# Optimization experiments

Measured on AMD Instinct MI355X. Metric: run time of the kernel, lower is better.

Reference implementation:

```python
import jax, jax.numpy as jnp
import numpy as np

B, T, C, H, M, R = 2, 2048, 768, 6, 3072, 320
D = C // H  # head_dim = 128


def setup_inputs() -> dict:
    key = jax.random.key(0)
    ks = jax.random.split(key, 11)
    s = 0.02
    return {
        "x": jax.random.normal(ks[0], (B, T, C), jnp.float32),
        "forward_memory": jax.random.normal(ks[1], (B, M, C), jnp.float32),
        "reverse_memory": jax.random.normal(ks[2], (B, R, C), jnp.float32),
        "ctrl": jax.random.uniform(ks[3], (5,), jnp.float32),
        "Wq": jax.random.normal(ks[4], (C, C), jnp.float32) * s,
        "Wk": jax.random.normal(ks[5], (C, C), jnp.float32) * s,
        "Wv": jax.random.normal(ks[6], (C, C), jnp.float32) * s,
        "Wo": jax.random.normal(ks[7], (C, C), jnp.float32) * s,
        "Wc": jax.random.normal(ks[8], (C, 5), jnp.float32) * 1e-4,  # ctrl_init_scale
        "Wg": jax.random.normal(ks[9], (H, C), jnp.float32) * s,
        "bg": jnp.full((H,), -1.0, jnp.float32),  # gate_bias_init
    }


def reference(x, forward_memory, reverse_memory, ctrl, Wq, Wk, Wv, Wo, Wc, Wg, bg):
    Bx, Tx, Cx = x.shape
    Hx = bg.shape[0]
    Dx = Cx // Hx
    # query with control-vector fusion (ctrl broadcast to every token)
    q = x @ Wq.T + ctrl @ Wc.T  # [B,T,C]
    # concat local tokens with forward+reverse memory, project K/V once
    kv_in = jnp.concatenate([x, forward_memory, reverse_memory], axis=1)  # [B,S,C]
    k = kv_in @ Wk.T
    v = kv_in @ Wv.T

    def heads(t):
        return t.reshape(Bx, -1, Hx, Dx).transpose(0, 2, 1, 3)  # [B,H,*,D]

    qh, kh, vh = heads(q), heads(k), heads(v)
    S = kh.shape[2]
    scores = jnp.einsum("bhtd,bhsd->bhts", qh, kh) * (Dx ** -0.5)
    # causal mask over local block only; memory columns always visible
    causal = jnp.triu(jnp.ones((Tx, Tx), bool), 1)
    mask = jnp.concatenate([causal, jnp.zeros((Tx, S - Tx), bool)], axis=1)
    scores = jnp.where(mask, jnp.float32(-1e30), scores)
    w = jax.nn.softmax(scores, axis=-1)  # [B,H,T,S]
    # split attention output into local and memory contributions
    local = jnp.einsum("bhts,bhsd->bhtd", w[..., :Tx], vh[:, :, :Tx])
    mem = jnp.einsum("bhts,bhsd->bhtd", w[..., Tx:], vh[:, :, Tx:])
    # per-head sigmoid gate on the memory path, computed from the fused query
    gate = jax.nn.sigmoid(q @ Wg.T + bg)  # [B,T,H]
    gate = gate.transpose(0, 2, 1)[..., None]  # [B,H,T,1]
    out = local + gate * mem
    out = out.transpose(0, 2, 1, 3).reshape(Bx, Tx, Cx)
    return out @ Wo.T
```

## Files before the change

### kernel.cpp

```cpp
#include <hip/hip_runtime.h>


typedef unsigned short u16;
typedef unsigned int   u32;
typedef __bf16 bf16x8 __attribute__((ext_vector_type(8)));
typedef float  f32x4  __attribute__((ext_vector_type(4)));

#define B_ 2
#define T_ 2048
#define C_ 768
#define H_ 6
#define D_ 128
#define M_ 3072
#define R_ 320
#define S_ 5440
#define BT_ 4096
#define BS_ 10880
#define NS_ 4
#define NMEM_ 53

#define GLDS(src, dst) __builtin_amdgcn_global_load_lds( \
    (const __attribute__((address_space(1))) void*)(src), \
    (__attribute__((address_space(3))) void*)(dst), 16, 0, 0)

#define MFMA16(a, b, c) __builtin_amdgcn_mfma_f32_16x16x32_bf16((a), (b), (c), 0, 0, 0)

__device__ __forceinline__ float b2f(u16 u) {
  union { u32 i; float f; } c; c.i = ((u32)u) << 16; return c.f;
}
__device__ __forceinline__ u16 f2b(float f) {
  union { float f; u32 i; } c; c.f = f;
  return (u16)((c.i + 0x7FFFu + ((c.i >> 16) & 1u)) >> 16);
}

__global__ __launch_bounds__(256) void k_cast4(const float* __restrict__ s0,
                                               const float* __restrict__ s1,
                                               const float* __restrict__ s2,
                                               const float* __restrict__ s3,
                                               u16* __restrict__ d0,
                                               u16* __restrict__ d1,
                                               u16* __restrict__ d2,
                                               u16* __restrict__ d3) {
  const float* src = (blockIdx.y == 0) ? s0 : (blockIdx.y == 1) ? s1
                   : (blockIdx.y == 2) ? s2 : s3;
  u16* dst = (blockIdx.y == 0) ? d0 : (blockIdx.y == 1) ? d1
           : (blockIdx.y == 2) ? d2 : d3;
  int i = (blockIdx.x * 256 + threadIdx.x) * 4;
  float4 v = *(const float4*)(src + i);
  u16 o[4] = { f2b(v.x), f2b(v.y), f2b(v.z), f2b(v.w) };
  *(ushort4*)(dst + i) = *(ushort4*)o;
}

__global__ __launch_bounds__(256) void k_concat(const float* __restrict__ x,
                                                const float* __restrict__ fm,
                                                const float* __restrict__ rm,
                                                u16* __restrict__ kv) {
  long long i = ((long long)blockIdx.x * 256 + threadIdx.x) * 8;
  if (i >= (long long)BS_ * C_) return;
  int row = (int)(i / C_);
  int col = (int)(i - (long long)row * C_);
  int b = row / S_, s = row - b * S_;
  const float* src;
  if (s < T_)           src = x  + (size_t)(b * T_ + s) * C_ + col;
  else if (s < T_ + M_) src = fm + (size_t)(b * M_ + (s - T_)) * C_ + col;
  else                  src = rm + (size_t)(b * R_ + (s - T_ - M_)) * C_ + col;
  float4 a0 = *(const float4*)src;
  float4 a1 = *(const float4*)(src + 4);
  u16 o[8] = { f2b(a0.x), f2b(a0.y), f2b(a0.z), f2b(a0.w),
               f2b(a1.x), f2b(a1.y), f2b(a1.z), f2b(a1.w) };
  *(uint4*)(kv + i) = *(uint4*)o;
}

template<bool F32OUT, bool QCBIAS>
__global__ __launch_bounds__(256) void k_gemm(const u16* __restrict__ A,
                                              const u16* __restrict__ W,
                                              const float* __restrict__ ctrl,
                                              const float* __restrict__ Wc,
                                              void* __restrict__ outv,
                                              int rows, int rowShift, int bstride) {
  __shared__ __align__(16) u16 As[3][128 * 32];
  __shared__ __align__(16) u16 Bs[3][128 * 32];
  const int t = threadIdx.x;
  const int lane = t & 63, wv = t >> 6;
  const int wr = (wv >> 1) * 64, wc = (wv & 1) * 64;
  const int fr = lane & 15, fq = lane >> 4;
  const int rowTile = blockIdx.x * 128;
  const int colTile = blockIdx.y * 128;

  f32x4 acc[4][4] = {};

  const int e0 = t * 8;
  const int e1 = (256 + t) * 8;
  const int r0 = e0 >> 5, c0 = e0 & 31;
  const int r1 = e1 >> 5, c1 = e1 & 31;

  int gr0 = rowTile + r0; if (gr0 >= rows) gr0 = rows - 1;
  int gr1 = rowTile + r1; if (gr1 >= rows) gr1 = rows - 1;
  const int msk = (1 << rowShift) - 1;
  const size_t pr0 = (size_t)(gr0 >> rowShift) * bstride + (gr0 & msk);
  const size_t pr1 = (size_t)(gr1 >> rowShift) * bstride + (gr1 & msk);
  const u16* gaB0 = A + pr0 * C_ + c0;
  const u16* gaB1 = A + pr1 * C_ + c1;
  const u16* gbB0 = W + (size_t)(colTile + r0) * C_ + c0;
  const u16* gbB1 = W + (size_t)(colTile + r1) * C_ + c1;
  const int aOff0 = (wv * 64) * 8, aOff1 = (256 + wv * 64) * 8;

#define STAGE_G(bi, kt) do { \
    GLDS(gaB0 + (kt), &As[bi][aOff0]); \
    GLDS(gaB1 + (kt), &As[bi][aOff1]); \
    GLDS(gbB0 + (kt), &Bs[bi][aOff0]); \
    GLDS(gbB1 + (kt), &Bs[bi][aOff1]); } while (0)

  STAGE_G(0, 0);
  STAGE_G(1, 32);
  int cur = 0;

  for (int kt = 0; kt < C_; kt += 32) {
    int nx2 = cur + 2; if (nx2 >= 3) nx2 -= 3;
    if (kt + 64 < C_) {
      STAGE_G(nx2, kt + 64);
      asm volatile("s_waitcnt vmcnt(8)" ::: "memory");
    } else if (kt + 32 < C_) {
      asm volatile("s_waitcnt vmcnt(4)" ::: "memory");
    } else {
      asm volatile("s_waitcnt vmcnt(0)" ::: "memory");
    }
    __builtin_amdgcn_s_barrier();

    bf16x8 af[4], bfr[4];
#pragma unroll
    for (int i = 0; i < 4; ++i) af[i]  = *(const bf16x8*)&As[cur][(wr + i * 16 + fr) * 32 + fq * 8];
#pragma unroll
    for (int i = 0; i < 4; ++i) bfr[i] = *(const bf16x8*)&Bs[cur][(wc + i * 16 + fr) * 32 + fq * 8];
#pragma unroll
    for (int mi = 0; mi < 4; ++mi)
#pragma unroll
      for (int ni = 0; ni < 4; ++ni)
        acc[mi][ni] = MFMA16(af[mi], bfr[ni], acc[mi][ni]);
    __builtin_amdgcn_s_barrier();
    cur = (cur == 2) ? 0 : cur + 1;
  }
#undef STAGE_G

#pragma unroll
  for (int mi = 0; mi < 4; ++mi) {
#pragma unroll
    for (int ni = 0; ni < 4; ++ni) {
      int cc = colTile + wc + ni * 16 + fr;
      float bb = 0.f;
      if (QCBIAS) {
#pragma unroll
        for (int j = 0; j < 5; ++j) bb += ctrl[j] * Wc[cc * 5 + j];
      }
#pragma unroll
      for (int j = 0; j < 4; ++j) {
        int rr = rowTile + wr + mi * 16 + fq * 4 + j;
        if (rr < rows) {
          float val = acc[mi][ni][j] + bb;
          if (F32OUT) ((float*)outv)[(size_t)rr * C_ + cc] = val;
          else        ((u16*)outv)[(size_t)rr * C_ + cc] = f2b(val);
        }
      }
    }
  }
}

__global__ __launch_bounds__(256, 2) void k_gemmKV(const u16* __restrict__ kvb,
                                                   const u16* __restrict__ Wk,
                                                   const u16* __restrict__ Wv,
                                                   u16* __restrict__ kb,
                                                   u16* __restrict__ vt) {
  __shared__ __align__(16) u16 As[2][128 * 32];
  __shared__ __align__(16) u16 Ks2[2][128 * 32];
  __shared__ __align__(16) u16 Vs2[2][128 * 32];
  const int t = threadIdx.x;
  const int lane = t & 63, wv = t >> 6;
  const int wr = (wv >> 1) * 64, wc = (wv & 1) * 64;
  const int fr = lane & 15, fq = lane >> 4;
  const int rowTile = blockIdx.x * 128;
  const int colTile = blockIdx.y * 128;

  f32x4 accK[4][4] = {};
  f32x4 accV[4][4] = {};

  const int e0 = t * 8;
  const int e1 = (256 + t) * 8;
  const int r0 = e0 >> 5, c0 = e0 & 31;
  const int r1 = e1 >> 5, c1 = e1 & 31;

  const u16* gaB0 = kvb + (size_t)(rowTile + r0) * C_ + c0;
  const u16* gaB1 = kvb + (size_t)(rowTile + r1) * C_ + c1;
  const u16* gkB0 = Wk + (size_t)(colTile + r0) * C_ + c0;
  const u16* gkB1 = Wk + (size_t)(colTile + r1) * C_ + c1;
  const u16* gvB0 = Wv + (size_t)(colTile + r0) * C_ + c0;
  const u16* gvB1 = Wv + (size_t)(colTile + r1) * C_ + c1;
  const int aOff0 = (wv * 64) * 8, aOff1 = (256 + wv * 64) * 8;

#define STAGE_KV(bi, kt) do { \
    GLDS(gaB0 + (kt), &As[bi][aOff0]); \
    GLDS(gaB1 + (kt), &As[bi][aOff1]); \
    GLDS(gkB0 + (kt), &Ks2[bi][aOff0]); \
    GLDS(gkB1 + (kt), &Ks2[bi][aOff1]); \
    GLDS(gvB0 + (kt), &Vs2[bi][aOff0]); \
    GLDS(gvB1 + (kt), &Vs2[bi][aOff1]); } while (0)

  STAGE_KV(0, 0);
  int cur = 0;

  for (int kt = 0; kt < C_; kt += 32) {
    if (kt + 32 < C_) {
      STAGE_KV(cur ^ 1, kt + 32);
      asm volatile("s_waitcnt vmcnt(6)" ::: "memory");
    } else {
      asm volatile("s_waitcnt vmcnt(0)" ::: "memory");
    }
    __builtin_amdgcn_s_barrier();

    bf16x8 af[4], wkf[4], wvf[4];
#pragma unroll
    for (int i = 0; i < 4; ++i) af[i]  = *(const bf16x8*)&As[cur][(wr + i * 16 + fr) * 32 + fq * 8];
#pragma unroll
    for (int i = 0; i < 4; ++i) wkf[i] = *(const bf16x8*)&Ks2[cur][(wc + i * 16 + fr) * 32 + fq * 8];
#pragma unroll
    for (int i = 0; i < 4; ++i) wvf[i] = *(const bf16x8*)&Vs2[cur][(wc + i * 16 + fr) * 32 + fq * 8];
#pragma unroll
    for (int mi = 0; mi < 4; ++mi)
#pragma unroll
      for (int ni = 0; ni < 4; ++ni) {
        accK[mi][ni] = MFMA16(af[mi], wkf[ni], accK[mi][ni]);
        accV[mi][ni] = MFMA16(wvf[mi], af[ni], accV[mi][ni]);
      }
    __builtin_amdgcn_s_barrier();
    cur ^= 1;
  }
#undef STAGE_KV

#pragma unroll
  for (int mi = 0; mi < 4; ++mi) {
#pragma unroll
    for (int ni = 0; ni < 4; ++ni) {
      int cc = colTile + wc + ni * 16 + fr;
#pragma unroll
      for (int j = 0; j < 4; ++j) {
        int rr = rowTile + wr + mi * 16 + fq * 4 + j;
        kb[(size_t)rr * C_ + cc] = f2b(accK[mi][ni][j]);
      }
    }
  }
#pragma unroll
  for (int mi = 0; mi < 4; ++mi) {
#pragma unroll
    for (int ni = 0; ni < 4; ++ni) {
      int sg = rowTile + wr + ni * 16 + fr;
      int b = sg / S_, s = sg - b * S_;
#pragma unroll
      for (int j = 0; j < 4; ++j) {
        int cc = colTile + wc + mi * 16 + fq * 4 + j;
        vt[((size_t)(b * C_ + cc)) * S_ + s] = f2b(accV[mi][ni][j]);
      }
    }
  }
}

__global__ __launch_bounds__(256) void k_gate(const u16* __restrict__ q,
                                              const float* __restrict__ Wg,
                                              const float* __restrict__ bg,
                                              float* __restrict__ gate) {
  int gid = blockIdx.x * 4 + (threadIdx.x >> 6);
  int lane = threadIdx.x & 63;
  int h = gid % H_;
  int bt = gid / H_;
  const u16* qrow = q + (size_t)bt * C_;
  const float* wrow = Wg + (size_t)h * C_;
  float a = 0.f;
#pragma unroll
  for (int i = 0; i < 12; ++i) {
    int e = i * 64 + lane;
    a += b2f(qrow[e]) * wrow[e];
  }
#pragma unroll
  for (int off = 1; off < 64; off <<= 1) a += __shfl_xor(a, off);
  if (lane == 0) {
    float xg = a + bg[h];
    int b = bt / T_, tt = bt - b * T_;
    gate[((size_t)b * H_ + h) * T_ + tt] = 1.f / (1.f + __expf(-xg));
  }
}

__global__ __launch_bounds__(256, 2) void k_attn10(const u16* __restrict__ q,
                                                   const u16* __restrict__ kk,
                                                   const u16* __restrict__ vt,
                                                   const float* __restrict__ gate,
                                                   u16* __restrict__ pacc0,
                                                   u16* __restrict__ pacc1,
                                                   u16* __restrict__ pacc2,
                                                   u16* __restrict__ pacc3,
                                                   float* __restrict__ pl) {
  __shared__ __align__(16) u16 Ks[2][64 * 128];
  __shared__ __align__(16) u16 Vs[128 * 64];
  __shared__ __align__(16) u16 Pb[4][32 * 64];

  const int bh = blockIdx.x;
  const int b = bh / H_, h = bh - b * H_;
  const int y = 15 - blockIdx.y;
  const int c = blockIdx.z;
  const int wv = threadIdx.x >> 6, lane = threadIdx.x & 63;
  const int fr = lane & 15, fq = lane >> 4;
  const int qbase = y * 128 + wv * 32;
  char* Pc = (char*)Pb[wv];

  const u16* Qh = q + (size_t)(b * T_ + qbase) * C_ + h * D_;
  const float* gh = gate + ((size_t)b * H_ + h) * T_ + qbase;

  const int kR = lane >> 4, kCb = (lane & 15) * 16;
  const u16* kS[4];
#pragma unroll
  for (int j = 0; j < 4; ++j) {
    int row = wv * 16 + j * 4 + kR;
    kS[j] = kk + (size_t)(b * S_ + row) * C_ + h * D_ + ((kCb ^ ((row & 7) << 4)) >> 1);
  }
  const int vR = lane >> 3, vCb = (lane & 7) * 16;
  const u16* vS[4];
#pragma unroll
  for (int j = 0; j < 4; ++j) {
    int row = wv * 32 + j * 8 + vR;
    vS[j] = vt + ((size_t)b * C_ + h * D_ + row) * S_ + ((vCb ^ ((row & 7) << 4)) >> 1);
  }

#define STAGE_K(buf, s) do { _Pragma("unroll") \
    for (int j = 0; j < 4; ++j) \
      GLDS(kS[j] + (size_t)(s) * C_, &Ks[buf][(wv * 16 + j * 4) * 128]); } while (0)
#define STAGE_V(s) do { _Pragma("unroll") \
    for (int j = 0; j < 4; ++j) \
      GLDS(vS[j] + (s), &Vs[(wv * 32 + j * 8) * 64]); } while (0)

  bf16x8 qf0[4], qf1[4];
#pragma unroll
  for (int kc = 0; kc < 4; ++kc) {
    qf0[kc] = *(const bf16x8*)&Qh[(size_t)fr * C_ + kc * 32 + fq * 8];
    qf1[kc] = *(const bf16x8*)&Qh[(size_t)(16 + fr) * C_ + kc * 32 + fq * 8];
  }

  f32x4 acc0[8] = {}, acc1[8] = {};
  f32x4 accL0 = {}, accM0 = {}, accL1 = {}, accM1 = {};
  float g0[4], lg0[4], g1[4], lg1[4];
#pragma unroll
  for (int r = 0; r < 4; ++r) {
    g0[r] = gh[fq * 4 + r];      lg0[r] = __log2f(g0[r]);
    g1[r] = gh[16 + fq * 4 + r]; lg1[r] = __log2f(g1[r]);
  }

  const __bf16 one_h = (__bf16)1.0f;
  bf16x8 ones = { one_h, one_h, one_h, one_h, one_h, one_h, one_h, one_h };

  const float scl = 0.08838834764831845f * 1.4426950408889634f;
  const int xk = (fr & 7) << 4;

  const int nloc = 2 * y + 2;
  const int ntot = nloc + NMEM_;
  auto s_of = [&](int i) { return (i < nloc) ? i * 64 : T_ + (i - nloc) * 64; };

  STAGE_K(0, s_of(c));
  int cur = 0;

  for (int i = c; i < ntot; i += NS_) {
    const int s0 = s_of(i);
    const bool haveNext = (i + NS_ < ntot);
    STAGE_V(s0);
    if (haveNext) {
      STAGE_K(cur ^ 1, s_of(i + NS_));
      asm volatile("s_waitcnt vmcnt(8)" ::: "memory");
    } else {
      asm volatile("s_waitcnt vmcnt(4)" ::: "memory");
    }
    __builtin_amdgcn_s_barrier();

    const bool loc = (i < nloc);
    const bool maskedStep = loc && (s0 + 63 > qbase);
    const bool skip = loc && (s0 > qbase + 31);

    bf16x8 pa00, pa01, pa10, pa11;
    if (!skip) {
      f32x4 sc0[4] = {{}, {}, {}, {}};
      f32x4 sc1[4] = {{}, {}, {}, {}};
#pragma unroll
      for (int quad = 0; quad < 4; ++quad) {
        const u16* Krow = &Ks[cur][(quad * 16 + fr) * 128];
#pragma unroll
        for (int kc = 0; kc < 4; ++kc) {
          bf16x8 kf = *(const bf16x8*)&Krow[((kc * 64 + fq * 16) ^ xk) >> 1];
          sc0[quad] = MFMA16(qf0[kc], kf, sc0[quad]);
          sc1[quad] = MFMA16(qf1[kc], kf, sc1[quad]);
        }
      }
      if (maskedStep) {
#pragma unroll
        for (int quad = 0; quad < 4; ++quad)
#pragma unroll
          for (int r = 0; r < 4; ++r) {
            int col = s0 + quad * 16 + fr;
            if (col > qbase + fq * 4 + r)      sc0[quad][r] = -1.0e30f;
            if (col > qbase + 16 + fq * 4 + r) sc1[quad][r] = -1.0e30f;
          }
      }
#pragma unroll
      for (int quad = 0; quad < 4; ++quad)
#pragma unroll
        for (int r = 0; r < 4; ++r) {
          int row = fq * 4 + r;
          int cb = (quad * 32 + fr * 2) ^ ((row & 7) << 4);
          float ca0 = loc ? 0.f : lg0[r];
          float ca1 = loc ? 0.f : lg1[r];
          *(__bf16*)(Pc + row * 128 + cb) =
              (__bf16)exp2f(fmaf(sc0[quad][r], scl, ca0));
          *(__bf16*)(Pc + (16 + row) * 128 + cb) =
              (__bf16)exp2f(fmaf(sc1[quad][r], scl, ca1));
        }
      __builtin_amdgcn_wave_barrier();
      pa00 = *(const bf16x8*)(Pc + fr * 128 + ((fq * 16) ^ xk));
      pa01 = *(const bf16x8*)(Pc + fr * 128 + ((64 + fq * 16) ^ xk));
      pa10 = *(const bf16x8*)(Pc + (16 + fr) * 128 + ((fq * 16) ^ xk));
      pa11 = *(const bf16x8*)(Pc + (16 + fr) * 128 + ((64 + fq * 16) ^ xk));
    }
    if (haveNext) asm volatile("s_waitcnt vmcnt(4)" ::: "memory");
    else          asm volatile("s_waitcnt vmcnt(0)" ::: "memory");
    __builtin_amdgcn_s_barrier();
    if (!skip) {
#pragma unroll
      for (int nt = 0; nt < 8; ++nt) {
        const u16* Vrow = &Vs[(nt * 16 + fr) * 64];
        bf16x8 vf0 = *(const bf16x8*)&Vrow[((fq * 16) ^ xk) >> 1];
        bf16x8 vf1 = *(const bf16x8*)&Vrow[((64 + fq * 16) ^ xk) >> 1];
        acc0[nt] = MFMA16(pa00, vf0, acc0[nt]);
        acc0[nt] = MFMA16(pa01, vf1, acc0[nt]);
        acc1[nt] = MFMA16(pa10, vf0, acc1[nt]);
        acc1[nt] = MFMA16(pa11, vf1, acc1[nt]);
      }
      if (loc) {
        accL0 = MFMA16(pa00, ones, accL0);
        accL0 = MFMA16(pa01, ones, accL0);
        accL1 = MFMA16(pa10, ones, accL1);
        accL1 = MFMA16(pa11, ones, accL1);
      } else {
        accM0 = MFMA16(pa00, ones, accM0);
        accM0 = MFMA16(pa01, ones, accM0);
        accM1 = MFMA16(pa10, ones, accM1);
        accM1 = MFMA16(pa11, ones, accM1);
      }
    }
    __builtin_amdgcn_s_barrier();
    cur ^= 1;
  }
#undef STAGE_K
#undef STAGE_V

  u16* pb = (c == 0) ? pacc0 : (c == 1) ? pacc1 : (c == 2) ? pacc2 : pacc3;
  const size_t rowb = (size_t)bh * T_ + qbase;
#pragma unroll
  for (int nt = 0; nt < 8; ++nt)
#pragma unroll
    for (int r = 0; r < 4; ++r) {
      ((__bf16*)pb)[(rowb + fq * 4 + r) * D_ + nt * 16 + fr] = (__bf16)acc0[nt][r];
      ((__bf16*)pb)[(rowb + 16 + fq * 4 + r) * D_ + nt * 16 + fr] = (__bf16)acc1[nt][r];
    }
  if (fr == 0) {
    const size_t plb = ((size_t)c * (B_ * H_) + bh) * T_ + qbase;
#pragma unroll
    for (int r = 0; r < 4; ++r) {
      pl[plb + fq * 4 + r]      = accL0[r] + accM0[r] / g0[r];
      pl[plb + 16 + fq * 4 + r] = accL1[r] + accM1[r] / g1[r];
    }
  }
}

__global__ __launch_bounds__(256) void k_combine(const u16* __restrict__ pacc0,
                                                 const u16* __restrict__ pacc1,
                                                 const u16* __restrict__ pacc2,
                                                 const u16* __restrict__ pacc3,
                                                 const float* __restrict__ pl,
                                                 u16* __restrict__ ao) {
  const int row = blockIdx.x * 4 + (threadIdx.x >> 6);
  const int lane = threadIdx.x & 63;
  const int bh = row >> 11, t = row & (T_ - 1);
  const int b = bh / H_, h = bh - b * H_;

  float L = pl[(size_t)bh * T_ + t]
          + pl[((size_t)(B_ * H_) + bh) * T_ + t]
          + pl[((size_t)(2 * B_ * H_) + bh) * T_ + t]
          + pl[((size_t)(3 * B_ * H_) + bh) * T_ + t];
  float inv = 1.f / L;
  const size_t rb = ((size_t)bh * T_ + t) * D_ + lane * 2;
  u32 v0 = *(const u32*)&pacc0[rb];
  u32 v1 = *(const u32*)&pacc1[rb];
  u32 v2 = *(const u32*)&pacc2[rb];
  u32 v3 = *(const u32*)&pacc3[rb];
  float o0 = b2f((u16)(v0 & 0xFFFF)) + b2f((u16)(v1 & 0xFFFF))
           + b2f((u16)(v2 & 0xFFFF)) + b2f((u16)(v3 & 0xFFFF));
  float o1 = b2f((u16)(v0 >> 16)) + b2f((u16)(v1 >> 16))
           + b2f((u16)(v2 >> 16)) + b2f((u16)(v3 >> 16));
  u16 o[2] = { f2b(o0 * inv), f2b(o1 * inv) };
  *(u32*)&ao[((size_t)(b * T_ + t)) * C_ + h * D_ + lane * 2] = *(u32*)o;
}

extern "C" void kernel_launch(void* const* d_in, const int* in_sizes, int n_in,
                              void* d_out, int out_size, void* d_ws, size_t ws_size,
                              hipStream_t stream) {
  const float* x   = (const float*)d_in[0];
  const float* fm  = (const float*)d_in[1];
  const float* rm  = (const float*)d_in[2];
  const float* ctl = (const float*)d_in[3];
  const float* Wq  = (const float*)d_in[4];
  const float* Wk  = (const float*)d_in[5];
  const float* Wv  = (const float*)d_in[6];
  const float* Wo  = (const float*)d_in[7];
  const float* Wc  = (const float*)d_in[8];
  const float* Wg  = (const float*)d_in[9];
  const float* bg  = (const float*)d_in[10];
  float* outp = (float*)d_out;

  char* ws = (char*)d_ws;
  float* gate = (float*)(ws + 4096);
  u16* qb    = (u16*)(ws + 102400);
  u16* kv    = (u16*)(ws + 6393856);
  u16* pacc0 = (u16*)(ws + 6393856);
  u16* pacc1 = (u16*)(ws + 12685312);
  u16* kb    = (u16*)(ws + 23105536);
  u16* vt    = (u16*)(ws + 39817216);
  u16* ao    = (u16*)(ws + 39817216);
  u16* pacc2 = (u16*)(ws + 56528896);
  u16* pacc3 = (u16*)(ws + 62820352);
  float* pl  = (float*)(ws + 69111808);
  u16* Wqb   = (u16*)(ws + 69505024);
  u16* Wkb   = (u16*)(ws + 70684672);
  u16* Wvb   = (u16*)(ws + 71864320);
  u16* Wob   = (u16*)(ws + 73043968);

  k_cast4<<<dim3(576, 4), dim3(256), 0, stream>>>(Wq, Wk, Wv, Wo,
                                                  Wqb, Wkb, Wvb, Wob);
  k_concat<<<dim3(4080), dim3(256), 0, stream>>>(x, fm, rm, kv);
  k_gemm<false, true><<<dim3(32, 6), dim3(256), 0, stream>>>(
      kv, Wqb, ctl, Wc, qb, BT_, 11, S_);
  k_gemmKV<<<dim3(85, 6), dim3(256), 0, stream>>>(kv, Wkb, Wvb, kb, vt);
  k_gate<<<dim3(6144), dim3(256), 0, stream>>>(qb, Wg, bg, gate);
  k_attn10<<<dim3(B_ * H_, 16, NS_), dim3(256), 0, stream>>>(
      qb, kb, vt, gate, pacc0, pacc1, pacc2, pacc3, pl);
  k_combine<<<dim3(6144), dim3(256), 0, stream>>>(pacc0, pacc1, pacc2, pacc3, pl, ao);
  k_gemm<true, false><<<dim3(32, 6), dim3(256), 0, stream>>>(
      ao, Wob, nullptr, nullptr, outp, BT_, 30, 0);
}
```

Measured before the change: 206.2 us.

## Load V fragments directly from global into registers instead of staging through LDS

New measurement: 338.0 us. +63.9%, slower.

```diff
diff --git a/kernel.cpp b/kernel.cpp
--- a/kernel.cpp
+++ b/kernel.cpp
@@ -287,7 +287,7 @@
   }
 }
 
-__global__ __launch_bounds__(256, 2) void k_attn10(const u16* __restrict__ q,
+__global__ __launch_bounds__(256, 2) void k_attn11(const u16* __restrict__ q,
                                                    const u16* __restrict__ kk,
                                                    const u16* __restrict__ vt,
                                                    const float* __restrict__ gate,
@@ -297,7 +297,6 @@
                                                    u16* __restrict__ pacc3,
                                                    float* __restrict__ pl) {
   __shared__ __align__(16) u16 Ks[2][64 * 128];
-  __shared__ __align__(16) u16 Vs[128 * 64];
   __shared__ __align__(16) u16 Pb[4][32 * 64];
 
   const int bh = blockIdx.x;
@@ -319,20 +318,11 @@
     int row = wv * 16 + j * 4 + kR;
     kS[j] = kk + (size_t)(b * S_ + row) * C_ + h * D_ + ((kCb ^ ((row & 7) << 4)) >> 1);
   }
-  const int vR = lane >> 3, vCb = (lane & 7) * 16;
-  const u16* vS[4];
-#pragma unroll
-  for (int j = 0; j < 4; ++j) {
-    int row = wv * 32 + j * 8 + vR;
-    vS[j] = vt + ((size_t)b * C_ + h * D_ + row) * S_ + ((vCb ^ ((row & 7) << 4)) >> 1);
-  }
+  const u16* vG = vt + ((size_t)b * C_ + h * D_ + fr) * S_ + fq * 8;
 
 #define STAGE_K(buf, s) do { _Pragma("unroll") \
     for (int j = 0; j < 4; ++j) \
       GLDS(kS[j] + (size_t)(s) * C_, &Ks[buf][(wv * 16 + j * 4) * 128]); } while (0)
-#define STAGE_V(s) do { _Pragma("unroll") \
-    for (int j = 0; j < 4; ++j) \
-      GLDS(vS[j] + (s), &Vs[(wv * 32 + j * 8) * 64]); } while (0)
 
   bf16x8 qf0[4], qf1[4];
 #pragma unroll
@@ -366,23 +356,29 @@
   for (int i = c; i < ntot; i += NS_) {
     const int s0 = s_of(i);
     const bool haveNext = (i + NS_ < ntot);
-    STAGE_V(s0);
-    if (haveNext) {
-      STAGE_K(cur ^ 1, s_of(i + NS_));
-      asm volatile("s_waitcnt vmcnt(8)" ::: "memory");
-    } else {
-      asm volatile("s_waitcnt vmcnt(4)" ::: "memory");
-    }
-    __builtin_amdgcn_s_barrier();
-
     const bool loc = (i < nloc);
     const bool maskedStep = loc && (s0 + 63 > qbase);
     const bool skip = loc && (s0 > qbase + 31);
 
-    bf16x8 pa00, pa01, pa10, pa11;
+    bf16x8 vfa[8], vfb[8];
     if (!skip) {
-      f32x4 sc0[4] = {{}, {}, {}, {}};
-      f32x4 sc1[4] = {{}, {}, {}, {}};
+#pragma unroll
+      for (int nt = 0; nt < 8; ++nt) {
+        vfa[nt] = *(const bf16x8*)&vG[(size_t)(nt * 16) * S_ + s0];
+        vfb[nt] = *(const bf16x8*)&vG[(size_t)(nt * 16) * S_ + s0 + 32];
+      }
+    }
+    if (haveNext) {
+      STAGE_K(cur ^ 1, s_of(i + NS_));
+      asm volatile("s_waitcnt vmcnt(20)" ::: "memory");
+    } else {
+      asm volatile("s_waitcnt vmcnt(16)" ::: "memory");
+    }
+    __builtin_amdgcn_s_barrier();
+
+    f32x4 sc0[4] = {{}, {}, {}, {}};
+    f32x4 sc1[4] = {{}, {}, {}, {}};
+    if (!skip) {
 #pragma unroll
       for (int quad = 0; quad < 4; ++quad) {
         const u16* Krow = &Ks[cur][(quad * 16 + fr) * 128];
@@ -393,6 +389,9 @@
           sc1[quad] = MFMA16(qf1[kc], kf, sc1[quad]);
         }
       }
+    }
+    __builtin_amdgcn_s_barrier();
+    if (!skip) {
       if (maskedStep) {
 #pragma unroll
         for (int quad = 0; quad < 4; ++quad)
@@ -417,24 +416,18 @@
               (__bf16)exp2f(fmaf(sc1[quad][r], scl, ca1));
         }
       __builtin_amdgcn_wave_barrier();
-      pa00 = *(const bf16x8*)(Pc + fr * 128 + ((fq * 16) ^ xk));
-      pa01 = *(const bf16x8*)(Pc + fr * 128 + ((64 + fq * 16) ^ xk));
-      pa10 = *(const bf16x8*)(Pc + (16 + fr) * 128 + ((fq * 16) ^ xk));
-      pa11 = *(const bf16x8*)(Pc + (16 + fr) * 128 + ((64 + fq * 16) ^ xk));
-    }
-    if (haveNext) asm volatile("s_waitcnt vmcnt(4)" ::: "memory");
-    else          asm volatile("s_waitcnt vmcnt(0)" ::: "memory");
-    __builtin_amdgcn_s_barrier();
-    if (!skip) {
+      bf16x8 pa00 = *(const bf16x8*)(Pc + fr * 128 + ((fq * 16) ^ xk));
+      bf16x8 pa01 = *(const bf16x8*)(Pc + fr * 128 + ((64 + fq * 16) ^ xk));
+      bf16x8 pa10 = *(const bf16x8*)(Pc + (16 + fr) * 128 + ((fq * 16) ^ xk));
+      bf16x8 pa11 = *(const bf16x8*)(Pc + (16 + fr) * 128 + ((64 + fq * 16) ^ xk));
+      if (haveNext) asm volatile("s_waitcnt vmcnt(4)" ::: "memory");
+      else          asm volatile("s_waitcnt vmcnt(0)" ::: "memory");
 #pragma unroll
       for (int nt = 0; nt < 8; ++nt) {
-        const u16* Vrow = &Vs[(nt * 16 + fr) * 64];
-        bf16x8 vf0 = *(const bf16x8*)&Vrow[((fq * 16) ^ xk) >> 1];
-        bf16x8 vf1 = *(const bf16x8*)&Vrow[((64 + fq * 16) ^ xk) >> 1];
-        acc0[nt] = MFMA16(pa00, vf0, acc0[nt]);
-        acc0[nt] = MFMA16(pa01, vf1, acc0[nt]);
-        acc1[nt] = MFMA16(pa10, vf0, acc1[nt]);
-        acc1[nt] = MFMA16(pa11, vf1, acc1[nt]);
+        acc0[nt] = MFMA16(pa00, vfa[nt], acc0[nt]);
+        acc0[nt] = MFMA16(pa01, vfb[nt], acc0[nt]);
+        acc1[nt] = MFMA16(pa10, vfa[nt], acc1[nt]);
+        acc1[nt] = MFMA16(pa11, vfb[nt], acc1[nt]);
       }
       if (loc) {
         accL0 = MFMA16(pa00, ones, accL0);
@@ -448,11 +441,9 @@
         accM1 = MFMA16(pa11, ones, accM1);
       }
     }
-    __builtin_amdgcn_s_barrier();
     cur ^= 1;
   }
 #undef STAGE_K
-#undef STAGE_V
 
   u16* pb = (c == 0) ? pacc0 : (c == 1) ? pacc1 : (c == 2) ? pacc2 : pacc3;
   const size_t rowb = (size_t)bh * T_ + qbase;
@@ -542,7 +533,7 @@
       kv, Wqb, ctl, Wc, qb, BT_, 11, S_);
   k_gemmKV<<<dim3(85, 6), dim3(256), 0, stream>>>(kv, Wkb, Wvb, kb, vt);
   k_gate<<<dim3(6144), dim3(256), 0, stream>>>(qb, Wg, bg, gate);
-  k_attn10<<<dim3(B_ * H_, 16, NS_), dim3(256), 0, stream>>>(
+  k_attn11<<<dim3(B_ * H_, 16, NS_), dim3(256), 0, stream>>>(
       qb, kb, vt, gate, pacc0, pacc1, pacc2, pacc3, pl);
   k_combine<<<dim3(6144), dim3(256), 0, stream>>>(pacc0, pacc1, pacc2, pacc3, pl, ao);
   k_gemm<true, false><<<dim3(32, 6), dim3(256), 0, stream>>>(
```
